# Kernel optimization log

Hardware: AMD Instinct MI355X
Metric: run time of the kernel (lower is better)

## Reference

```python
import jax, jax.numpy as jnp
import numpy as np

WIN = 9  # local window size per spatial dim

def _boxfilter3d(x):
    k = jnp.ones((1, 1, WIN, WIN, WIN), x.dtype) / float(WIN ** 3)
    return jax.lax.conv_general_dilated(
        x, k, window_strides=(1, 1, 1), padding='SAME',
        dimension_numbers=('NCDHW', 'OIDHW', 'NCDHW'))

def setup_inputs() -> dict:
    key = jax.random.key(0)
    k1, k2 = jax.random.split(key)
    shape = (2, 1, 160, 192, 160)
    y_true = jax.random.uniform(k1, shape, dtype=jnp.float32)
    y_pred = jax.random.uniform(k2, shape, dtype=jnp.float32)
    return {"y_true": y_true, "y_pred": y_pred}

def reference(y_true, y_pred):
    Ii, Ji = y_true, y_pred
    mu1 = _boxfilter3d(Ii)
    mu2 = _boxfilter3d(Ji)
    sigma1_sq = _boxfilter3d(Ii * Ii) - mu1 * mu1
    sigma2_sq = _boxfilter3d(Ji * Ji) - mu2 * mu2
    sigma12 = _boxfilter3d(Ii * Ji) - mu1 * mu2
    cc = (sigma12 * sigma12) / (sigma1_sq * sigma2_sq + 1e-5)
    return -jnp.mean(cc)
```

## Files before the change

kernel.cpp:

```cpp
#include <hip/hip_runtime.h>

#define DD 160
#define HH 192
#define WW 160
#define HWs (HH * WW)
#define NTOT 9830400.0f
#define DOUT 20
#define NIT  28
#define NBLK 960

#define SDS 11
#define SDC (24 * SDS + 1)
#define SDP (5 * SDC)
#define HSS 11
#define HSC (16 * HSS + 1)
#define HSP (5 * HSC)

typedef float    v4 __attribute__((ext_vector_type(4)));
typedef _Float16 h4 __attribute__((ext_vector_type(4)));

__device__ __forceinline__ void block_sync_lds() {
    __builtin_amdgcn_s_waitcnt(0xc07f);
    __builtin_amdgcn_s_barrier();
}
__device__ __forceinline__ v4 up(h4 x) { return __builtin_convertvector(x, v4); }
__device__ __forceinline__ h4 dn(v4 x) { return __builtin_convertvector(x, h4); }

__global__ __launch_bounds__(256, 4) void kf(const float* __restrict__ I,
                                             const float* __restrict__ J,
                                             float* __restrict__ partial) {
    __shared__ h4    SDL[2 * SDP];
    __shared__ h4    HSL[2 * HSP];
    __shared__ float red[256];

    const int tid = threadIdx.x;
    const int bx = blockIdx.x, by = blockIdx.y, b = blockIdx.z;
    const int w0 = (bx % 5) * 32, h0 = (bx / 5) * 16;
    const int d0 = by * DOUT;
    const int bid = bx + 60 * (by + 8 * b);

    const int rt = tid ^ ((bx & 1) << 7);

    const bool p1 = rt < 240;
    const int r = rt / 10, g = rt % 10;
    const int gh = h0 - 4 + r, gw = w0 - 4 + g * 4;
    const bool colOK = p1 && gh >= 0 && gh < HH && gw >= 0 && gw < WW;
    const size_t colOff = (size_t)gh * WW + gw;
    const float* Ib = I + (size_t)b * DD * HWs + colOff;
    const float* Jb = J + (size_t)b * DD * HWs + colOff;
    h4* const sdw = &SDL[r * SDS + g];

    const bool p2 = rt < 100;
    const int g2 = rt % 10, ch2 = (rt / 10) % 5, hh0 = (rt / 50) * 8;
    const int sdrOff = ch2 * SDC + hh0 * SDS + g2;
    const int hswOff = ch2 * HSC + hh0 * HSS + g2;

    const bool p3 = rt >= 128;
    const int q3 = rt & 127;
    const int hh = q3 >> 3, sg = q3 & 7;
    const int hsrOff = hh * HSS + sg;

    v4 sd0 = 0.f, sd1 = 0.f, sd2 = 0.f, sd3 = 0.f, sd4 = 0.f;
    h4 fI[9], fJ[9];
#pragma unroll
    for (int u = 0; u < 9; ++u) { fI[u] = (h4)(_Float16)0; fJ[u] = (h4)(_Float16)0; }
    v4 pLI = 0.f, pLJ = 0.f;
    float acc = 0.f;
    const float inv = 1.0f / 729.0f;

    {
        const int si = d0 - 4;
        if (colOK && si >= 0) {
            pLI = *(const v4*)(Ib + (size_t)si * HWs);
            pLJ = *(const v4*)(Jb + (size_t)si * HWs);
        }
    }

    for (int tb = 0; tb < 36; tb += 9) {
#pragma unroll
        for (int u = 0; u < 9; ++u) {
            const int t = tb + u;
            if (t < NIT + 2) {
                if (t < NIT && p1) {
                    h4 cI = dn(pLI), cJ = dn(pLJ);
                    v4 aI = up(cI), aJ = up(cJ);
                    v4 dI = aI, dJv = aJ;
                    v4 dII = aI * aI, dJJ = aJ * aJ, dIJ = aI * aJ;
                    if (t >= 9) {
                        v4 bI = up(fI[u]), bJ = up(fJ[u]);
                        dI -= bI; dJv -= bJ;
                        dII -= bI * bI; dJJ -= bJ * bJ; dIJ -= bI * bJ;
                    }
                    fI[u] = cI; fJ[u] = cJ;
                    sd0 += dI; sd1 += dJv; sd2 += dII; sd3 += dJJ; sd4 += dIJ;
                    h4* const sdq = sdw + (t & 1) * SDP;
                    sdq[0]       = dn(sd0);
                    sdq[SDC]     = dn(sd1);
                    sdq[2 * SDC] = dn(sd2);
                    sdq[3 * SDC] = dn(sd3);
                    sdq[4 * SDC] = dn(sd4);
                    pLI = 0.f; pLJ = 0.f;
                    const int sn = d0 - 3 + t;
                    if (t + 1 < NIT && colOK && sn >= 0 && sn < DD) {
                        pLI = *(const v4*)(Ib + (size_t)sn * HWs);
                        pLJ = *(const v4*)(Jb + (size_t)sn * HWs);
                    }
                }

                if (t >= 1 && t <= NIT && p2) {
                    const int par = (t - 1) & 1;
                    const h4* const sdr = &SDL[par * SDP + sdrOff];
                    h4* const hsw = &HSL[par * HSP + hswOff];
                    h4 s = sdr[0];
#pragma unroll
                    for (int k = 1; k < 9; ++k) s += sdr[k * SDS];
                    hsw[0] = s;
#pragma unroll
                    for (int j = 1; j < 8; ++j) {
                        s += sdr[(j + 8) * SDS] - sdr[(j - 1) * SDS];
                        hsw[j * HSS] = s;
                    }
                }

                if (t >= 10 && p3) {
                    const h4* const hsr = &HSL[(t & 1) * HSP + hsrOff];
                    float w[5][4];
#pragma unroll
                    for (int c = 0; c < 5; ++c) {
                        v4 fa = up(hsr[c * HSC]);
                        v4 fb = up(hsr[c * HSC + 1]);
                        v4 fc = up(hsr[c * HSC + 2]);
                        float s = fa[0] + fa[1] + fa[2] + fa[3] +
                                  fb[0] + fb[1] + fb[2] + fb[3] + fc[0];
                        w[c][0] = s;
                        s += fc[1] - fa[0]; w[c][1] = s;
                        s += fc[2] - fa[1]; w[c][2] = s;
                        s += fc[3] - fa[2]; w[c][3] = s;
                    }
#pragma unroll
                    for (int e = 0; e < 4; ++e) {
                        float mu1 = w[0][e] * inv, mu2 = w[1][e] * inv;
                        float g1  = fmaf(-mu1, mu1, w[2][e] * inv);
                        float g2v = fmaf(-mu2, mu2, w[3][e] * inv);
                        float g12 = fmaf(-mu1, mu2, w[4][e] * inv);
                        acc += __fdividef(g12 * g12, fmaf(g1, g2v, 1e-5f));
                    }
                }

                block_sync_lds();
            }
        }
    }

    red[tid] = acc;
    __syncthreads();
    if (tid < 128) red[tid] += red[tid + 128];
    __syncthreads();
    if (tid < 64) {
        float a = red[tid] + red[tid + 64];
#pragma unroll
        for (int off = 32; off > 0; off >>= 1) a += __shfl_down(a, off);
        if (tid == 0) partial[bid] = a;
    }
}

__global__ void k3_final(const float* __restrict__ partial,
                         float* __restrict__ out) {
    __shared__ float r[1024];
    const int i = threadIdx.x;
    r[i] = (i < NBLK) ? partial[i] : 0.f;
    __syncthreads();
    for (int off = 512; off > 0; off >>= 1) {
        if (i < off) r[i] += r[i + off];
        __syncthreads();
    }
    if (i == 0) out[0] = -r[0] * (1.0f / NTOT);
}

extern "C" void kernel_launch(void* const* d_in, const int* in_sizes, int n_in,
                              void* d_out, int out_size, void* d_ws, size_t ws_size,
                              hipStream_t stream) {
    (void)in_sizes; (void)n_in; (void)out_size; (void)ws_size;
    const float* I = (const float*)d_in[0];
    const float* J = (const float*)d_in[1];
    float* out     = (float*)d_out;
    float* partial = (float*)d_ws;

    dim3 grid(60, 8, 2);
    kf<<<grid, 256, 0, stream>>>(I, J, partial);
    k3_final<<<1, 1024, 0, stream>>>(partial, out);
}
```

Before: 148.3 us.

## Rebalance warp roles, deepen load prefetch, and compute depth deltas in fp16

The depth-slab deltas and their squares are now computed in packed half precision instead of fp32, and the global prefetch is two slices deep instead of one. The H-direction sliding-sum stage is reassigned so 50 threads each scan a full 16-row column, keeping a register ring of the last nine slices instead of reloading from LDS. The W-stage threads are remapped to 64..191 and the LDS channel pitches are changed to new padded values. These aim to cut ALU and LDS work, hide load latency, and spread work across the wavefronts. The cost is more registers and lower precision in the squared terms, which could change rounding error.

```diff
diff --git a/kernel.cpp b/kernel.cpp
--- a/kernel.cpp
+++ b/kernel.cpp
@@ -10,10 +10,10 @@
 #define NBLK 960
 
 #define SDS 11
-#define SDC (24 * SDS + 1)
+#define SDC 266
 #define SDP (5 * SDC)
 #define HSS 11
-#define HSC (16 * HSS + 1)
+#define HSC 186
 #define HSP (5 * HSC)
 
 typedef float    v4 __attribute__((ext_vector_type(4)));
@@ -50,31 +50,38 @@
     const float* Jb = J + (size_t)b * DD * HWs + colOff;
     h4* const sdw = &SDL[r * SDS + g];
 
-    const bool p2 = rt < 100;
-    const int g2 = rt % 10, ch2 = (rt / 10) % 5, hh0 = (rt / 50) * 8;
-    const int sdrOff = ch2 * SDC + hh0 * SDS + g2;
-    const int hswOff = ch2 * HSC + hh0 * HSS + g2;
-
-    const bool p3 = rt >= 128;
-    const int q3 = rt & 127;
-    const int hh = q3 >> 3, sg = q3 & 7;
-    const int hsrOff = hh * HSS + sg;
+    const bool p3 = (rt >= 64) && (rt < 192);
+    const int q3 = rt - 64;
+    const int hh = q3 & 15, e3 = q3 >> 4;
+    const int hsrOff = hh * HSS + e3;
+
+    const bool p2 = (rt >= 192) && (rt < 242);
+    const int u2 = rt - 192;
+    const int c2 = u2 / 10, g2 = u2 % 10;
+    const int sdrOff = c2 * SDC + g2;
+    const int hswOff = c2 * HSC + g2;
 
     v4 sd0 = 0.f, sd1 = 0.f, sd2 = 0.f, sd3 = 0.f, sd4 = 0.f;
     h4 fI[9], fJ[9];
 #pragma unroll
     for (int u = 0; u < 9; ++u) { fI[u] = (h4)(_Float16)0; fJ[u] = (h4)(_Float16)0; }
-    v4 pLI = 0.f, pLJ = 0.f;
+
+    v4 pAI = 0.f, pAJ = 0.f, pBI = 0.f, pBJ = 0.f;
+    {
+        const int s0 = d0 - 4;
+        if (colOK && s0 >= 0) {
+            pAI = *(const v4*)(Ib + (size_t)s0 * HWs);
+            pAJ = *(const v4*)(Jb + (size_t)s0 * HWs);
+        }
+        const int s1 = d0 - 3;
+        if (colOK && s1 >= 0) {
+            pBI = *(const v4*)(Ib + (size_t)s1 * HWs);
+            pBJ = *(const v4*)(Jb + (size_t)s1 * HWs);
+        }
+    }
+
     float acc = 0.f;
     const float inv = 1.0f / 729.0f;
-
-    {
-        const int si = d0 - 4;
-        if (colOK && si >= 0) {
-            pLI = *(const v4*)(Ib + (size_t)si * HWs);
-            pLJ = *(const v4*)(Jb + (size_t)si * HWs);
-        }
-    }
 
     for (int tb = 0; tb < 36; tb += 9) {
 #pragma unroll
@@ -82,43 +89,29 @@
             const int t = tb + u;
             if (t < NIT + 2) {
                 if (t < NIT && p1) {
-                    h4 cI = dn(pLI), cJ = dn(pLJ);
-                    v4 aI = up(cI), aJ = up(cJ);
-                    v4 dI = aI, dJv = aJ;
-                    v4 dII = aI * aI, dJJ = aJ * aJ, dIJ = aI * aJ;
+                    h4 cI = dn(pAI), cJ = dn(pAJ);
+                    h4 dI = cI, dJ = cJ;
+                    h4 dII = cI * cI, dJJ = cJ * cJ, dIJ = cI * cJ;
                     if (t >= 9) {
-                        v4 bI = up(fI[u]), bJ = up(fJ[u]);
-                        dI -= bI; dJv -= bJ;
-                        dII -= bI * bI; dJJ -= bJ * bJ; dIJ -= bI * bJ;
+                        h4 oI = fI[u], oJ = fJ[u];
+                        dI -= oI; dJ -= oJ;
+                        dII -= oI * oI; dJJ -= oJ * oJ; dIJ -= oI * oJ;
                     }
                     fI[u] = cI; fJ[u] = cJ;
-                    sd0 += dI; sd1 += dJv; sd2 += dII; sd3 += dJJ; sd4 += dIJ;
+                    sd0 += up(dI); sd1 += up(dJ); sd2 += up(dII);
+                    sd3 += up(dJJ); sd4 += up(dIJ);
                     h4* const sdq = sdw + (t & 1) * SDP;
                     sdq[0]       = dn(sd0);
                     sdq[SDC]     = dn(sd1);
                     sdq[2 * SDC] = dn(sd2);
                     sdq[3 * SDC] = dn(sd3);
                     sdq[4 * SDC] = dn(sd4);
-                    pLI = 0.f; pLJ = 0.f;
-                    const int sn = d0 - 3 + t;
-                    if (t + 1 < NIT && colOK && sn >= 0 && sn < DD) {
-                        pLI = *(const v4*)(Ib + (size_t)sn * HWs);
-                        pLJ = *(const v4*)(Jb + (size_t)sn * HWs);
-                    }
-                }
-
-                if (t >= 1 && t <= NIT && p2) {
-                    const int par = (t - 1) & 1;
-                    const h4* const sdr = &SDL[par * SDP + sdrOff];
-                    h4* const hsw = &HSL[par * HSP + hswOff];
-                    h4 s = sdr[0];
-#pragma unroll
-                    for (int k = 1; k < 9; ++k) s += sdr[k * SDS];
-                    hsw[0] = s;
-#pragma unroll
-                    for (int j = 1; j < 8; ++j) {
-                        s += sdr[(j + 8) * SDS] - sdr[(j - 1) * SDS];
-                        hsw[j * HSS] = s;
+                    pAI = pBI; pAJ = pBJ;
+                    pBI = 0.f; pBJ = 0.f;
+                    const int sn = d0 - 2 + t;
+                    if (t + 2 < NIT && colOK && sn >= 0 && sn < DD) {
+                        pBI = *(const v4*)(Ib + (size_t)sn * HWs);
+                        pBJ = *(const v4*)(Jb + (size_t)sn * HWs);
                     }
                 }
 
@@ -147,6 +140,29 @@
                     }
                 }
 
+                if (t >= 1 && t <= NIT && p2) {
+                    const int par = (t - 1) & 1;
+                    const h4* const sdr = &SDL[par * SDP + sdrOff];
+                    h4* const hsw = &HSL[par * HSP + hswOff];
+                    h4 win[9];
+                    h4 s;
+                    win[0] = sdr[0]; s = win[0];
+#pragma unroll
+                    for (int k = 1; k < 9; ++k) {
+                        win[k] = sdr[k * SDS];
+                        s += win[k];
+                    }
+                    hsw[0] = s;
+#pragma unroll
+                    for (int j = 1; j < 16; ++j) {
+                        h4 nv = sdr[(j + 8) * SDS];
+                        const int slot = (j - 1) % 9;
+                        s += nv - win[slot];
+                        win[slot] = nv;
+                        hsw[j * HSS] = s;
+                    }
+                }
+
                 block_sync_lds();
             }
         }
```

Measured after the change: 152.1 us. 2.6% more time.
